# Kernel optimization log

Measured on AMD Instinct MI355X. Metric: run time of the kernel, lower is better.

Reference implementation:

```python
import jax, jax.numpy as jnp
import numpy as np
from jax import lax

RADIUS = 8
EPS = 0.01


def box_filter(x, r):
    # Sum over a (2r+1)x(2r+1) window with zero ('same') padding — identical math
    # to depthwise conv2d with a ones kernel and padding=r.
    k = 2 * r + 1
    return lax.reduce_window(
        x, jnp.array(0, x.dtype), lax.add,
        window_dimensions=(1, 1, k, k),
        window_strides=(1, 1, 1, 1),
        padding=((0, 0), (0, 0), (r, r), (r, r)),
    )


def setup_inputs() -> dict:
    key = jax.random.key(0)
    k1, k2 = jax.random.split(key)
    shape = (16, 3, 512, 512)
    I = jax.random.uniform(k1, shape, dtype=jnp.float32)
    p = jax.random.uniform(k2, shape, dtype=jnp.float32)
    return {"I": I, "p": p}


def reference(I, p):
    r = RADIUS
    eps = EPS
    N = box_filter(jnp.ones_like(I), r)          # window pixel counts (handles borders)
    mean_I = box_filter(I, r) / N
    mean_p = box_filter(p, r) / N
    mean_Ip = box_filter(I * p, r) / N
    cov_Ip = mean_Ip - mean_I * mean_p
    mean_II = box_filter(I * I, r) / N
    var_I = mean_II - mean_I * mean_I
    a = cov_Ip / (var_I + eps)
    b = mean_p - a * mean_I
    mean_a = box_filter(a, r) / N
    mean_b = box_filter(b, r) / N
    q = mean_a * I + mean_b
    return q
```

## Files before the change

### kernel.cpp

```cpp
#include <hip/hip_runtime.h>


#define RAD  8
#define H    512
#define W    512
#define TILE 32
#define EPS  0.01f

__global__ __launch_bounds__(512, 4)
void guided_filter_kernel(const float* __restrict__ Ig,
                          const float* __restrict__ Pg,
                          float* __restrict__ out)
{
    __shared__ __align__(16) char smem_lo[32768];
    __shared__ float4 H4[64 * 48];

    float2* F2  = (float2*)smem_lo;
    float2* AB  = (float2*)smem_lo;
    float2* HAB = (float2*)(smem_lo + 18816);

    const int tid   = threadIdx.x;
    const int plane = blockIdx.z;
    const int x0 = blockIdx.x * TILE - 2 * RAD;
    const int y0 = blockIdx.y * TILE - 2 * RAD;
    const float* Ib = Ig + (size_t)plane * (H * W);
    const float* Pb = Pg + (size_t)plane * (H * W);
    float* Ob = out + (size_t)plane * (H * W);

    const bool interior = (x0 >= 0) && (y0 >= 0) && (x0 + 64 <= W) && (y0 + 64 <= H);
    if (interior) {
        #pragma unroll
        for (int it = 0; it < 2; ++it) {
            int idx = it * 512 + tid;
            int ry = idx >> 4, f4 = idx & 15;
            const float* ip = Ib + (y0 + ry) * W + x0 + 4 * f4;
            const float* pp = Pb + (y0 + ry) * W + x0 + 4 * f4;
            float4 iv = *(const float4*)ip;
            float4 pv = *(const float4*)pp;
            int pc = (4 * f4 + 4 * ry) & 63;
            float2* dst = &F2[ry * 64 + pc];
            dst[0] = make_float2(iv.x, pv.x);
            dst[1] = make_float2(iv.y, pv.y);
            dst[2] = make_float2(iv.z, pv.z);
            dst[3] = make_float2(iv.w, pv.w);
        }
    } else {
        #pragma unroll
        for (int it = 0; it < 2; ++it) {
            int idx = it * 512 + tid;
            int ry = idx >> 4, f4 = idx & 15;
            int gy = y0 + ry;
            int pc = (4 * f4 + 4 * ry) & 63;
            float2* dst = &F2[ry * 64 + pc];
            #pragma unroll
            for (int k = 0; k < 4; ++k) {
                int gx = x0 + 4 * f4 + k;
                bool v = ((unsigned)gy < (unsigned)H) && ((unsigned)gx < (unsigned)W);
                float a = v ? Ib[gy * W + gx] : 0.f;
                float b = v ? Pb[gy * W + gx] : 0.f;
                dst[k] = make_float2(a, b);
            }
        }
    }
    __syncthreads();

    {
        int r = tid >> 3, e = tid & 7;
        const float2* Frow = &F2[r * 64];
        const int rot = 4 * r;
        const int c0 = 6 * e;
        float4 S = make_float4(0.f, 0.f, 0.f, 0.f);
        #pragma unroll
        for (int j = 0; j < 17; ++j) {
            float2 v = Frow[(c0 + j + rot) & 63];
            S.x += v.x; S.y += v.y; S.z += v.x * v.y; S.w += v.x * v.x;
        }
        #pragma unroll
        for (int k = 0; k < 6; ++k) {
            H4[r * 48 + c0 + k] = S;
            if (k < 5) {
                float2 va = Frow[(c0 + k + 17 + rot) & 63];
                float2 vs = Frow[(c0 + k + rot) & 63];
                S.x += va.x - vs.x;
                S.y += va.y - vs.y;
                S.z += va.x * va.y - vs.x * vs.y;
                S.w += va.x * va.x - vs.x * vs.x;
            }
        }
    }
    __syncthreads();

    if (tid < 384) {
        int col   = tid % 48;
        int chunk = tid / 48;
        int cy0   = chunk * 6;
        float4 S = make_float4(0.f, 0.f, 0.f, 0.f);
        #pragma unroll
        for (int j = 0; j < 17; ++j) {
            float4 v = H4[(cy0 + j) * 48 + col];
            S.x += v.x; S.y += v.y; S.z += v.z; S.w += v.w;
        }
        int gx = x0 + RAD + col;
        int nx = min(gx + RAD, W - 1) - max(gx - RAD, 0) + 1;
        #pragma unroll
        for (int k = 0; k < 6; ++k) {
            int cy = cy0 + k;
            int gy = y0 + RAD + cy;
            float a = 0.f, b = 0.f;
            if (((unsigned)gy < (unsigned)H) && ((unsigned)gx < (unsigned)W)) {
                int ny = min(gy + RAD, H - 1) - max(gy - RAD, 0) + 1;
                float invN = 1.f / (float)(nx * ny);
                float mI = S.x * invN, mp = S.y * invN;
                float cov = S.z * invN - mI * mp;
                float var = S.w * invN - mI * mI;
                a = cov / (var + EPS);
                b = mp - a * mI;
            }
            AB[cy * 49 + col] = make_float2(a, b);
            if (k < 5) {
                float4 va = H4[(cy + 17) * 48 + col];
                float4 vs = H4[cy * 48 + col];
                S.x += va.x - vs.x; S.y += va.y - vs.y;
                S.z += va.z - vs.z; S.w += va.w - vs.w;
            }
        }
    }
    __syncthreads();

    if (tid < 384) {
        int r = tid % 48;
        int e = tid / 48;
        const float2* row = &AB[r * 49];
        const int c0 = 4 * e;
        float2 S = make_float2(0.f, 0.f);
        #pragma unroll
        for (int j = 0; j < 17; ++j) {
            float2 v = row[c0 + j];
            S.x += v.x; S.y += v.y;
        }
        #pragma unroll
        for (int k = 0; k < 4; ++k) {
            HAB[r * 33 + c0 + k] = S;
            if (k < 3) {
                float2 va = row[c0 + k + 17];
                float2 vs = row[c0 + k];
                S.x += va.x - vs.x; S.y += va.y - vs.y;
            }
        }
    }
    __syncthreads();

    {
        int col   = tid & 31;
        int chunk = tid >> 5;
        int oy0   = chunk * 2;
        float2 S = make_float2(0.f, 0.f);
        #pragma unroll
        for (int j = 0; j < 17; ++j) {
            float2 v = HAB[(oy0 + j) * 33 + col];
            S.x += v.x; S.y += v.y;
        }
        int gx = x0 + 2 * RAD + col;
        int nx = min(gx + RAD, W - 1) - max(gx - RAD, 0) + 1;
        #pragma unroll
        for (int k = 0; k < 2; ++k) {
            int oy = oy0 + k;
            int gy = y0 + 2 * RAD + oy;
            int ny = min(gy + RAD, H - 1) - max(gy - RAD, 0) + 1;
            float invN = 1.f / (float)(nx * ny);
            float iv = Ib[gy * W + gx];
            Ob[gy * W + gx] = S.x * invN * iv + S.y * invN;
            if (k < 1) {
                float2 va = HAB[(oy + 17) * 33 + col];
                float2 vs = HAB[oy * 33 + col];
                S.x += va.x - vs.x; S.y += va.y - vs.y;
            }
        }
    }
}

extern "C" void kernel_launch(void* const* d_in, const int* in_sizes, int n_in,
                              void* d_out, int out_size, void* d_ws, size_t ws_size,
                              hipStream_t stream) {
    const float* I = (const float*)d_in[0];
    const float* P = (const float*)d_in[1];
    float* out = (float*)d_out;
    int planes = in_sizes[0] / (H * W);
    dim3 grid(W / TILE, H / TILE, planes);
    guided_filter_kernel<<<grid, dim3(512), 0, stream>>>(I, P, out);
}
```

Baseline: 257.9 us.

## Swizzle shared-memory layouts with XOR and widen LDS reads to float4

Replaces the rotated float2 staging layout with an XOR-swizzled float4 layout, so the horizontal box-sum initial window can be read as paired float4 loads. The H4 intermediate is XOR-swizzled per row, and the AB stride is padded to 50 so that the horizontal pass over AB can also use float4 reads. These changes are meant to cut LDS bank conflicts and the number of LDS instructions. Exact divisions are replaced with hardware reciprocal approximations, which trades a small amount of precision for cheaper arithmetic.

Result: faster. 248.1 us (-3.8%).

```diff
diff --git a/kernel.cpp b/kernel.cpp
--- a/kernel.cpp
+++ b/kernel.cpp
@@ -12,12 +12,12 @@
                           const float* __restrict__ Pg,
                           float* __restrict__ out)
 {
-    __shared__ __align__(16) char smem_lo[32768];
-    __shared__ float4 H4[64 * 48];
-
-    float2* F2  = (float2*)smem_lo;
-    float2* AB  = (float2*)smem_lo;
-    float2* HAB = (float2*)(smem_lo + 18816);
+    __shared__ __align__(16) float4 F4[64 * 32];
+    __shared__ __align__(16) float4 H4[64 * 48];
+
+    float2* F2p = (float2*)F4;
+    float2* AB  = (float2*)F4;
+    float2* HAB = (float2*)F4 + 48 * 50;
 
     const int tid   = threadIdx.x;
     const int plane = blockIdx.z;
@@ -33,54 +33,71 @@
         for (int it = 0; it < 2; ++it) {
             int idx = it * 512 + tid;
             int ry = idx >> 4, f4 = idx & 15;
+            int rl = ry & 7, pf = ry & 1;
             const float* ip = Ib + (y0 + ry) * W + x0 + 4 * f4;
             const float* pp = Pb + (y0 + ry) * W + x0 + 4 * f4;
             float4 iv = *(const float4*)ip;
             float4 pv = *(const float4*)pp;
-            int pc = (4 * f4 + 4 * ry) & 63;
-            float2* dst = &F2[ry * 64 + pc];
-            dst[0] = make_float2(iv.x, pv.x);
-            dst[1] = make_float2(iv.y, pv.y);
-            dst[2] = make_float2(iv.z, pv.z);
-            dst[3] = make_float2(iv.w, pv.w);
+            float2 e0 = make_float2(iv.x, pv.x), e1 = make_float2(iv.y, pv.y);
+            float2 e2 = make_float2(iv.z, pv.z), e3 = make_float2(iv.w, pv.w);
+            float2 a0 = pf ? e1 : e0, a1 = pf ? e0 : e1;
+            float2 b0 = pf ? e3 : e2, b1 = pf ? e2 : e3;
+            float4* Fr = &F4[ry * 32];
+            Fr[(2 * f4) ^ rl]     = make_float4(a0.x, a0.y, a1.x, a1.y);
+            Fr[(2 * f4 + 1) ^ rl] = make_float4(b0.x, b0.y, b1.x, b1.y);
         }
     } else {
         #pragma unroll
         for (int it = 0; it < 2; ++it) {
             int idx = it * 512 + tid;
             int ry = idx >> 4, f4 = idx & 15;
+            int rl = ry & 7, pf = ry & 1;
             int gy = y0 + ry;
-            int pc = (4 * f4 + 4 * ry) & 63;
-            float2* dst = &F2[ry * 64 + pc];
+            float2 el[4];
             #pragma unroll
             for (int k = 0; k < 4; ++k) {
                 int gx = x0 + 4 * f4 + k;
                 bool v = ((unsigned)gy < (unsigned)H) && ((unsigned)gx < (unsigned)W);
-                float a = v ? Ib[gy * W + gx] : 0.f;
-                float b = v ? Pb[gy * W + gx] : 0.f;
-                dst[k] = make_float2(a, b);
-            }
+                el[k].x = v ? Ib[gy * W + gx] : 0.f;
+                el[k].y = v ? Pb[gy * W + gx] : 0.f;
+            }
+            float2 a0 = pf ? el[1] : el[0], a1 = pf ? el[0] : el[1];
+            float2 b0 = pf ? el[3] : el[2], b1 = pf ? el[2] : el[3];
+            float4* Fr = &F4[ry * 32];
+            Fr[(2 * f4) ^ rl]     = make_float4(a0.x, a0.y, a1.x, a1.y);
+            Fr[(2 * f4 + 1) ^ rl] = make_float4(b0.x, b0.y, b1.x, b1.y);
         }
     }
     __syncthreads();
 
     {
-        int r = tid >> 3, e = tid & 7;
-        const float2* Frow = &F2[r * 64];
-        const int rot = 4 * r;
+        const int r  = tid >> 3, e = tid & 7;
+        const int rl = r & 7, pf = r & 1;
         const int c0 = 6 * e;
+        const float4* Fr = &F4[r * 32];
+        const float2* Er = &F2p[r * 64];
         float4 S = make_float4(0.f, 0.f, 0.f, 0.f);
-        #pragma unroll
-        for (int j = 0; j < 17; ++j) {
-            float2 v = Frow[(c0 + j + rot) & 63];
+        const int g0 = 3 * e;
+        #pragma unroll
+        for (int m = 0; m < 8; ++m) {
+            float4 g = Fr[(g0 + m) ^ rl];
+            S.x += g.x + g.z;
+            S.y += g.y + g.w;
+            S.z += g.x * g.y + g.z * g.w;
+            S.w += g.x * g.x + g.z * g.z;
+        }
+        {
+            int c = c0 + 16;
+            float2 v = Er[(((c >> 1) ^ rl) << 1) | pf];
             S.x += v.x; S.y += v.y; S.z += v.x * v.y; S.w += v.x * v.x;
         }
         #pragma unroll
         for (int k = 0; k < 6; ++k) {
-            H4[r * 48 + c0 + k] = S;
+            H4[r * 48 + ((c0 + k) ^ rl)] = S;
             if (k < 5) {
-                float2 va = Frow[(c0 + k + 17 + rot) & 63];
-                float2 vs = Frow[(c0 + k + rot) & 63];
+                int ca = c0 + k + 17, cs = c0 + k;
+                float2 va = Er[(((ca >> 1) ^ rl) << 1) | ((ca & 1) ^ pf)];
+                float2 vs = Er[(((cs >> 1) ^ rl) << 1) | ((cs & 1) ^ pf)];
                 S.x += va.x - vs.x;
                 S.y += va.y - vs.y;
                 S.z += va.x * va.y - vs.x * vs.y;
@@ -91,13 +108,13 @@
     __syncthreads();
 
     if (tid < 384) {
-        int col   = tid % 48;
-        int chunk = tid / 48;
-        int cy0   = chunk * 6;
+        const int col = tid % 48, chunk = tid / 48;
+        const int cy0 = chunk * 6;
         float4 S = make_float4(0.f, 0.f, 0.f, 0.f);
         #pragma unroll
         for (int j = 0; j < 17; ++j) {
-            float4 v = H4[(cy0 + j) * 48 + col];
+            int row = cy0 + j;
+            float4 v = H4[row * 48 + (col ^ (row & 7))];
             S.x += v.x; S.y += v.y; S.z += v.z; S.w += v.w;
         }
         int gx = x0 + RAD + col;
@@ -109,17 +126,18 @@
             float a = 0.f, b = 0.f;
             if (((unsigned)gy < (unsigned)H) && ((unsigned)gx < (unsigned)W)) {
                 int ny = min(gy + RAD, H - 1) - max(gy - RAD, 0) + 1;
-                float invN = 1.f / (float)(nx * ny);
+                float invN = __builtin_amdgcn_rcpf((float)(nx * ny));
                 float mI = S.x * invN, mp = S.y * invN;
                 float cov = S.z * invN - mI * mp;
                 float var = S.w * invN - mI * mI;
-                a = cov / (var + EPS);
+                a = cov * __builtin_amdgcn_rcpf(var + EPS);
                 b = mp - a * mI;
             }
-            AB[cy * 49 + col] = make_float2(a, b);
+            AB[cy * 50 + col] = make_float2(a, b);
             if (k < 5) {
-                float4 va = H4[(cy + 17) * 48 + col];
-                float4 vs = H4[cy * 48 + col];
+                int ra = cy + 17, rs = cy;
+                float4 va = H4[ra * 48 + (col ^ (ra & 7))];
+                float4 vs = H4[rs * 48 + (col ^ (rs & 7))];
                 S.x += va.x - vs.x; S.y += va.y - vs.y;
                 S.z += va.z - vs.z; S.w += va.w - vs.w;
             }
@@ -128,14 +146,19 @@
     __syncthreads();
 
     if (tid < 384) {
-        int r = tid % 48;
-        int e = tid / 48;
-        const float2* row = &AB[r * 49];
+        const int r = tid % 48, e = tid / 48;
         const int c0 = 4 * e;
+        const float2* row  = &AB[r * 50];
+        const float4* rowg = (const float4*)row;
         float2 S = make_float2(0.f, 0.f);
         #pragma unroll
-        for (int j = 0; j < 17; ++j) {
-            float2 v = row[c0 + j];
+        for (int m = 0; m < 8; ++m) {
+            float4 g = rowg[2 * e + m];
+            S.x += g.x + g.z;
+            S.y += g.y + g.w;
+        }
+        {
+            float2 v = row[c0 + 16];
             S.x += v.x; S.y += v.y;
         }
         #pragma unroll
@@ -151,9 +174,8 @@
     __syncthreads();
 
     {
-        int col   = tid & 31;
-        int chunk = tid >> 5;
-        int oy0   = chunk * 2;
+        const int col = tid & 31, chunk = tid >> 5;
+        const int oy0 = chunk * 2;
         float2 S = make_float2(0.f, 0.f);
         #pragma unroll
         for (int j = 0; j < 17; ++j) {
@@ -167,7 +189,7 @@
             int oy = oy0 + k;
             int gy = y0 + 2 * RAD + oy;
             int ny = min(gy + RAD, H - 1) - max(gy - RAD, 0) + 1;
-            float invN = 1.f / (float)(nx * ny);
+            float invN = __builtin_amdgcn_rcpf((float)(nx * ny));
             float iv = Ib[gy * W + gx];
             Ob[gy * W + gx] = S.x * invN * iv + S.y * invN;
             if (k < 1) {
```
